# Optimization experiments

Measured on AMD Instinct MI355X. Metric: run time of the kernel, lower is better.

The kernel has to match this reference:

```python
import jax, jax.numpy as jnp
import numpy as np

DIM = 256
HEADS = 8
SR = 2
EPS = 1e-5


def setup_inputs() -> dict:
    key = jax.random.key(0)
    ks = jax.random.split(key, 8)
    B, N, C = 4, 4096, DIM
    s = 0.02
    return {
        "x": jax.random.normal(ks[0], (B, N, C), dtype=jnp.float32),
        "H": 64,
        "W": 64,
        # sequence-reduction conv (Conv2d dim->dim, k=SR, stride=SR), OIHW
        "sr_w": jax.random.normal(ks[1], (C, C, SR, SR), dtype=jnp.float32) * s,
        "sr_b": jnp.zeros((C,), dtype=jnp.float32),
        "ln_g": jnp.ones((C,), dtype=jnp.float32),
        "ln_b": jnp.zeros((C,), dtype=jnp.float32),
        # torch Linear weights: y = x @ W.T (qkv_bias=False)
        "q_w": jax.random.normal(ks[2], (C, C), dtype=jnp.float32) * s,
        "kv_w": jax.random.normal(ks[3], (2 * C, C), dtype=jnp.float32) * s,
        "proj_w": jax.random.normal(ks[4], (C, C), dtype=jnp.float32) * s,
        "proj_b": jnp.zeros((C,), dtype=jnp.float32),
    }


def reference(x, H, W, sr_w, sr_b, ln_g, ln_b, q_w, kv_w, proj_w, proj_b):
    B, N, C = x.shape
    h, d = HEADS, C // HEADS
    scale = d ** -0.5

    # q: [B, h, N, d]
    q = (x @ q_w.T).reshape(B, N, h, d).transpose(0, 2, 1, 3)

    # sequence reduction: [B,N,C] -> [B,C,H,W] -> conv(k=SR, s=SR) -> [B, N', C]
    x_ = x.transpose(0, 2, 1).reshape(B, C, H, W)
    x_ = jax.lax.conv_general_dilated(
        x_, sr_w, window_strides=(SR, SR), padding="VALID",
        dimension_numbers=("NCHW", "OIHW", "NCHW"))
    x_ = x_ + sr_b[None, :, None, None]
    x_ = x_.reshape(B, C, -1).transpose(0, 2, 1)  # [B, N', C]

    # LayerNorm over C
    mu = x_.mean(-1, keepdims=True)
    var = x_.var(-1, keepdims=True)
    x_ = (x_ - mu) * jax.lax.rsqrt(var + EPS) * ln_g + ln_b

    # kv: [2, B, h, N', d]
    kv = (x_ @ kv_w.T).reshape(B, -1, 2, h, d).transpose(2, 0, 3, 1, 4)
    k, v = kv[0], kv[1]

    attn = jnp.einsum("bhnd,bhmd->bhnm", q, k) * scale
    attn = jax.nn.softmax(attn, axis=-1)  # attn_drop = 0 -> identity
    out = jnp.einsum("bhnm,bhmd->bhnd", attn, v)
    out = out.transpose(0, 2, 1, 3).reshape(B, N, C)

    return out @ proj_w.T + proj_b  # proj_drop = 0 -> identity
```

## Files before the change

kernel.cpp:

```cpp
#include <hip/hip_runtime.h>
#include <hip/hip_bf16.h>


typedef __attribute__((ext_vector_type(8))) short bf16x8;
typedef __attribute__((ext_vector_type(8))) unsigned short u16x8;
typedef __attribute__((ext_vector_type(4))) float f32x4;
typedef __attribute__((ext_vector_type(16))) float f32x16;
typedef __attribute__((ext_vector_type(2))) unsigned u32x2v;
typedef __attribute__((ext_vector_type(4))) unsigned u32x4v;

__device__ inline unsigned short f2bf(float f) {
  unsigned u = __float_as_uint(f);
  u += 0x7fffu + ((u >> 16) & 1u);
  return (unsigned short)(u >> 16);
}

__device__ inline u16x8 cast8(float4 a, float4 b) {
  u16x8 r;
  r[0] = f2bf(a.x); r[1] = f2bf(a.y); r[2] = f2bf(a.z); r[3] = f2bf(a.w);
  r[4] = f2bf(b.x); r[5] = f2bf(b.y); r[6] = f2bf(b.z); r[7] = f2bf(b.w);
  return r;
}

__global__ __launch_bounds__(256) void prep_kernel(
    const float* __restrict__ srw, unsigned short* __restrict__ srw_bf) {
  const int o = blockIdx.x, t = threadIdx.x;
  float4 v = reinterpret_cast<const float4*>(srw + (size_t)o * 1024)[t];
  srw_bf[(size_t)o * 1024 + 0 * 256 + t] = f2bf(v.x);
  srw_bf[(size_t)o * 1024 + 1 * 256 + t] = f2bf(v.y);
  srw_bf[(size_t)o * 1024 + 2 * 256 + t] = f2bf(v.z);
  srw_bf[(size_t)o * 1024 + 3 * 256 + t] = f2bf(v.w);
}

__device__ __forceinline__ void gemm_body_q(
    const float* __restrict__ Af, const float* __restrict__ W,
    unsigned short* __restrict__ C, float oscale,
    int m0, int n0, unsigned short* Asb, unsigned short* Bsb) {
  const int K = 256, N = 256, NK = 8;
  const int tid = threadIdx.x;
  const int w = tid >> 6, l = tid & 63, c = l & 15, g = l >> 4;
  const int wr = w >> 1, wc = w & 1;
  const int ar = tid >> 1, ah = tid & 1;
  const int bn = tid >> 2, bq = tid & 3;
  const int ABUF = 128 * 40, BBUF = 64 * 40;

  const float* aptr = Af + (size_t)(m0 + ar) * K + ah * 16;
  const float* wptr = W + (size_t)(n0 + bn) * K + bq * 8;

  f32x4 acc[4][2];
#pragma unroll
  for (int mt = 0; mt < 4; ++mt)
#pragma unroll
    for (int nt = 0; nt < 2; ++nt)
#pragma unroll
      for (int r = 0; r < 4; ++r) acc[mt][nt][r] = 0.f;

  {
    float4 a0 = *reinterpret_cast<const float4*>(aptr);
    float4 a1 = *reinterpret_cast<const float4*>(aptr + 4);
    float4 a2 = *reinterpret_cast<const float4*>(aptr + 8);
    float4 a3 = *reinterpret_cast<const float4*>(aptr + 12);
    float4 w0 = *reinterpret_cast<const float4*>(wptr);
    float4 w1 = *reinterpret_cast<const float4*>(wptr + 4);
    *reinterpret_cast<u16x8*>(&Asb[ar * 40 + ah * 16]) = cast8(a0, a1);
    *reinterpret_cast<u16x8*>(&Asb[ar * 40 + ah * 16 + 8]) = cast8(a2, a3);
    *reinterpret_cast<u16x8*>(&Bsb[bn * 40 + bq * 8]) = cast8(w0, w1);
  }

  for (int t = 0; t < NK; ++t) {
    const int cur = t & 1;
    __syncthreads();
    float4 na0, na1, na2, na3, nw0, nw1;
    if (t < NK - 1) {
      const float* ap = aptr + (t + 1) * 32;
      na0 = *reinterpret_cast<const float4*>(ap);
      na1 = *reinterpret_cast<const float4*>(ap + 4);
      na2 = *reinterpret_cast<const float4*>(ap + 8);
      na3 = *reinterpret_cast<const float4*>(ap + 12);
      const float* wp = wptr + (t + 1) * 32;
      nw0 = *reinterpret_cast<const float4*>(wp);
      nw1 = *reinterpret_cast<const float4*>(wp + 4);
    }
    bf16x8 af[4], bfr[2];
#pragma unroll
    for (int mt = 0; mt < 4; ++mt)
      af[mt] = *reinterpret_cast<const bf16x8*>(
          &Asb[cur * ABUF + (wr * 64 + mt * 16 + c) * 40 + g * 8]);
#pragma unroll
    for (int nt = 0; nt < 2; ++nt)
      bfr[nt] = *reinterpret_cast<const bf16x8*>(
          &Bsb[cur * BBUF + (wc * 32 + nt * 16 + c) * 40 + g * 8]);
#pragma unroll
    for (int mt = 0; mt < 4; ++mt)
#pragma unroll
      for (int nt = 0; nt < 2; ++nt)
        acc[mt][nt] = __builtin_amdgcn_mfma_f32_16x16x32_bf16(
            af[mt], bfr[nt], acc[mt][nt], 0, 0, 0);
    if (t < NK - 1) {
      const int nxt = cur ^ 1;
      *reinterpret_cast<u16x8*>(&Asb[nxt * ABUF + ar * 40 + ah * 16]) = cast8(na0, na1);
      *reinterpret_cast<u16x8*>(&Asb[nxt * ABUF + ar * 40 + ah * 16 + 8]) = cast8(na2, na3);
      *reinterpret_cast<u16x8*>(&Bsb[nxt * BBUF + bn * 40 + bq * 8]) = cast8(nw0, nw1);
    }
  }

#pragma unroll
  for (int mt = 0; mt < 4; ++mt)
#pragma unroll
    for (int nt = 0; nt < 2; ++nt) {
      int row = m0 + wr * 64 + mt * 16 + g * 4;
      int col = n0 + wc * 32 + nt * 16 + c;
#pragma unroll
      for (int r = 0; r < 4; ++r)
        C[(size_t)(row + r) * N + col] = f2bf(acc[mt][nt][r] * oscale);
    }
}

__device__ __forceinline__ void conv_body(
    const float* __restrict__ Xf, const unsigned short* __restrict__ Wp,
    const float* __restrict__ bias, float* __restrict__ C,
    int m0, int n0, unsigned short* Asb, unsigned short* Bsb) {
  const int NK = 32;
  const int tid = threadIdx.x;
  const int w = tid >> 6, l = tid & 63, c = l & 15, g = l >> 4;
  const int wr = w >> 1, wc = w & 1;
  const int sr = tid >> 2, sh = tid & 3;
  const int BUF = 64 * 40;

  int base[4];
  {
    int row = m0 + sr;
    int b = row >> 10, o = row & 1023, oh = o >> 5, ow = o & 31;
#pragma unroll
    for (int tap = 0; tap < 4; ++tap) {
      int n = ((oh << 1) + (tap >> 1)) * 64 + (ow << 1) + (tap & 1);
      base[tap] = ((b << 12) + n) << 8;
    }
  }
  const unsigned short* wptr = Wp + (size_t)(n0 + sr) * 1024 + sh * 8;

  f32x4 acc[2][2];
#pragma unroll
  for (int mt = 0; mt < 2; ++mt)
#pragma unroll
    for (int nt = 0; nt < 2; ++nt)
#pragma unroll
      for (int r = 0; r < 4; ++r) acc[mt][nt][r] = 0.f;

  {
    const float* xp = Xf + base[0] + sh * 8;
    float4 a0 = *reinterpret_cast<const float4*>(xp);
    float4 a1 = *reinterpret_cast<const float4*>(xp + 4);
    *reinterpret_cast<u16x8*>(&Asb[sr * 40 + sh * 8]) = cast8(a0, a1);
    *reinterpret_cast<u16x8*>(&Bsb[sr * 40 + sh * 8]) =
        *reinterpret_cast<const u16x8*>(wptr);
  }

  for (int t = 0; t < NK; ++t) {
    const int cur = t & 1;
    __syncthreads();
    float4 na0, na1; u16x8 nw;
    if (t < NK - 1) {
      const int k0n = (t + 1) * 32;
      const float* xp = Xf + base[k0n >> 8] + (k0n & 255) + sh * 8;
      na0 = *reinterpret_cast<const float4*>(xp);
      na1 = *reinterpret_cast<const float4*>(xp + 4);
      nw = *reinterpret_cast<const u16x8*>(wptr + (t + 1) * 32);
    }
    bf16x8 af[2], bfr[2];
#pragma unroll
    for (int mt = 0; mt < 2; ++mt)
      af[mt] = *reinterpret_cast<const bf16x8*>(
          &Asb[cur * BUF + (wr * 32 + mt * 16 + c) * 40 + g * 8]);
#pragma unroll
    for (int nt = 0; nt < 2; ++nt)
      bfr[nt] = *reinterpret_cast<const bf16x8*>(
          &Bsb[cur * BUF + (wc * 32 + nt * 16 + c) * 40 + g * 8]);
#pragma unroll
    for (int mt = 0; mt < 2; ++mt)
#pragma unroll
      for (int nt = 0; nt < 2; ++nt)
        acc[mt][nt] = __builtin_amdgcn_mfma_f32_16x16x32_bf16(
            af[mt], bfr[nt], acc[mt][nt], 0, 0, 0);
    if (t < NK - 1) {
      const int nxt = cur ^ 1;
      *reinterpret_cast<u16x8*>(&Asb[nxt * BUF + sr * 40 + sh * 8]) = cast8(na0, na1);
      *reinterpret_cast<u16x8*>(&Bsb[nxt * BUF + sr * 40 + sh * 8]) = nw;
    }
  }

#pragma unroll
  for (int mt = 0; mt < 2; ++mt)
#pragma unroll
    for (int nt = 0; nt < 2; ++nt) {
      int row = m0 + wr * 32 + mt * 16 + g * 4;
      int col = n0 + wc * 32 + nt * 16 + c;
      float bv = bias[col];
#pragma unroll
      for (int r = 0; r < 4; ++r)
        C[(size_t)(row + r) * 256 + col] = acc[mt][nt][r] + bv;
    }
}

__global__ __launch_bounds__(256) void qconv_kernel(
    const float* __restrict__ x, const float* __restrict__ q_w,
    unsigned short* __restrict__ q_bf, const unsigned short* __restrict__ srw_bf,
    const float* __restrict__ sr_b, float* __restrict__ xred, float qscale) {
  __shared__ unsigned short smem[2 * 128 * 40 + 2 * 64 * 40];
  const int bid = blockIdx.x;
  if (bid < 512) {
    gemm_body_q(x, q_w, q_bf, qscale,
                (bid >> 2) * 128, (bid & 3) * 64, smem, smem + 2 * 128 * 40);
  } else {
    int cb = bid - 512;
    conv_body(x, srw_bf, sr_b, xred,
              (cb >> 2) * 64, (cb & 3) * 64, smem, smem + 2 * 64 * 40);
  }
}

__global__ __launch_bounds__(256) void kv_gemm(
    const unsigned short* __restrict__ A, const float* __restrict__ W,
    unsigned short* __restrict__ Kb, unsigned short* __restrict__ Vtp) {
  __shared__ unsigned short Asb[2 * 128 * 40];
  __shared__ unsigned short Bsb[2 * 64 * 40];
  const int K = 256, NK = 8;
  const int tid = threadIdx.x;
  const int w = tid >> 6, l = tid & 63, c = l & 15, g = l >> 4;
  const int wr = w >> 1, wc = w & 1;
  const int m0 = blockIdx.y * 128, n0 = blockIdx.x * 64;
  const int ar = tid >> 1, ah = tid & 1;
  const int bn = tid >> 2, bq = tid & 3;
  const int ABUF = 128 * 40, BBUF = 64 * 40;

  const unsigned short* aptr = A + (size_t)(m0 + ar) * K + ah * 16;
  const float* wptr = W + (size_t)(n0 + bn) * K + bq * 8;

  f32x4 acc[4][2];
#pragma unroll
  for (int mt = 0; mt < 4; ++mt)
#pragma unroll
    for (int nt = 0; nt < 2; ++nt)
#pragma unroll
      for (int r = 0; r < 4; ++r) acc[mt][nt][r] = 0.f;

  {
    u16x8 a0 = *reinterpret_cast<const u16x8*>(aptr);
    u16x8 a1 = *reinterpret_cast<const u16x8*>(aptr + 8);
    float4 w0 = *reinterpret_cast<const float4*>(wptr);
    float4 w1 = *reinterpret_cast<const float4*>(wptr + 4);
    *reinterpret_cast<u16x8*>(&Asb[ar * 40 + ah * 16]) = a0;
    *reinterpret_cast<u16x8*>(&Asb[ar * 40 + ah * 16 + 8]) = a1;
    *reinterpret_cast<u16x8*>(&Bsb[bn * 40 + bq * 8]) = cast8(w0, w1);
  }

  for (int t = 0; t < NK; ++t) {
    const int cur = t & 1;
    __syncthreads();
    u16x8 na0, na1; float4 nw0, nw1;
    if (t < NK - 1) {
      const unsigned short* ap = aptr + (t + 1) * 32;
      na0 = *reinterpret_cast<const u16x8*>(ap);
      na1 = *reinterpret_cast<const u16x8*>(ap + 8);
      const float* wp = wptr + (t + 1) * 32;
      nw0 = *reinterpret_cast<const float4*>(wp);
      nw1 = *reinterpret_cast<const float4*>(wp + 4);
    }
    bf16x8 af[4], bfr[2];
#pragma unroll
    for (int mt = 0; mt < 4; ++mt)
      af[mt] = *reinterpret_cast<const bf16x8*>(
          &Asb[cur * ABUF + (wr * 64 + mt * 16 + c) * 40 + g * 8]);
#pragma unroll
    for (int nt = 0; nt < 2; ++nt)
      bfr[nt] = *reinterpret_cast<const bf16x8*>(
          &Bsb[cur * BBUF + (wc * 32 + nt * 16 + c) * 40 + g * 8]);
#pragma unroll
    for (int mt = 0; mt < 4; ++mt)
#pragma unroll
      for (int nt = 0; nt < 2; ++nt)
        acc[mt][nt] = __builtin_amdgcn_mfma_f32_16x16x32_bf16(
            af[mt], bfr[nt], acc[mt][nt], 0, 0, 0);
    if (t < NK - 1) {
      const int nxt = cur ^ 1;
      *reinterpret_cast<u16x8*>(&Asb[nxt * ABUF + ar * 40 + ah * 16]) = na0;
      *reinterpret_cast<u16x8*>(&Asb[nxt * ABUF + ar * 40 + ah * 16 + 8]) = na1;
      *reinterpret_cast<u16x8*>(&Bsb[nxt * BBUF + bn * 40 + bq * 8]) = cast8(nw0, nw1);
    }
  }

#pragma unroll
  for (int mt = 0; mt < 4; ++mt)
#pragma unroll
    for (int nt = 0; nt < 2; ++nt) {
      int row = m0 + wr * 64 + mt * 16 + g * 4;
      int col = n0 + wc * 32 + nt * 16 + c;
#pragma unroll
      for (int r = 0; r < 4; ++r) {
        float v = acc[mt][nt][r];
        if (col < 256) {
          Kb[(size_t)(row + r) * 256 + col] = f2bf(v);
        } else {
          int head = (col - 256) >> 5, d = (col - 256) & 31;
          int rr = row + r;
          Vtp[((size_t)(((rr >> 10) << 3) + head) * 32 + d) * 1024 +
              (rr & 1023)] = f2bf(v);
        }
      }
    }
}

__global__ __launch_bounds__(256) void proj_gemm(
    const unsigned short* __restrict__ A, const float* __restrict__ W,
    const float* __restrict__ bias, float* __restrict__ C) {
  __shared__ unsigned short Asb[2 * 64 * 40];
  __shared__ unsigned short Bsb[2 * 64 * 40];
  const int NK = 8;
  const int tid = threadIdx.x;
  const int w = tid >> 6, l = tid & 63, c = l & 15, g = l >> 4;
  const int wr = w >> 1, wc = w & 1;
  const int m0 = blockIdx.y * 64, n0 = blockIdx.x * 64;
  const int sr = tid >> 2, sh = tid & 3;
  const int BUF = 64 * 40;

  const unsigned short* aptr = A + (size_t)(m0 + sr) * 256 + sh * 8;
  const float* wptr = W + (size_t)(n0 + sr) * 256 + sh * 8;

  f32x4 acc[2][2];
#pragma unroll
  for (int mt = 0; mt < 2; ++mt)
#pragma unroll
    for (int nt = 0; nt < 2; ++nt)
#pragma unroll
      for (int r = 0; r < 4; ++r) acc[mt][nt][r] = 0.f;

  {
    u16x8 av = *reinterpret_cast<const u16x8*>(aptr);
    float4 w0 = *reinterpret_cast<const float4*>(wptr);
    float4 w1 = *reinterpret_cast<const float4*>(wptr + 4);
    *reinterpret_cast<u16x8*>(&Asb[sr * 40 + sh * 8]) = av;
    *reinterpret_cast<u16x8*>(&Bsb[sr * 40 + sh * 8]) = cast8(w0, w1);
  }

  for (int t = 0; t < NK; ++t) {
    const int cur = t & 1;
    __syncthreads();
    u16x8 na; float4 nw0, nw1;
    if (t < NK - 1) {
      na = *reinterpret_cast<const u16x8*>(aptr + (t + 1) * 32);
      const float* wp = wptr + (t + 1) * 32;
      nw0 = *reinterpret_cast<const float4*>(wp);
      nw1 = *reinterpret_cast<const float4*>(wp + 4);
    }
    bf16x8 af[2], bfr[2];
#pragma unroll
    for (int mt = 0; mt < 2; ++mt)
      af[mt] = *reinterpret_cast<const bf16x8*>(
          &Asb[cur * BUF + (wr * 32 + mt * 16 + c) * 40 + g * 8]);
#pragma unroll
    for (int nt = 0; nt < 2; ++nt)
      bfr[nt] = *reinterpret_cast<const bf16x8*>(
          &Bsb[cur * BUF + (wc * 32 + nt * 16 + c) * 40 + g * 8]);
#pragma unroll
    for (int mt = 0; mt < 2; ++mt)
#pragma unroll
      for (int nt = 0; nt < 2; ++nt)
        acc[mt][nt] = __builtin_amdgcn_mfma_f32_16x16x32_bf16(
            af[mt], bfr[nt], acc[mt][nt], 0, 0, 0);
    if (t < NK - 1) {
      const int nxt = cur ^ 1;
      *reinterpret_cast<u16x8*>(&Asb[nxt * BUF + sr * 40 + sh * 8]) = na;
      *reinterpret_cast<u16x8*>(&Bsb[nxt * BUF + sr * 40 + sh * 8]) = cast8(nw0, nw1);
    }
  }

#pragma unroll
  for (int mt = 0; mt < 2; ++mt)
#pragma unroll
    for (int nt = 0; nt < 2; ++nt) {
      int row = m0 + wr * 32 + mt * 16 + g * 4;
      int col = n0 + wc * 32 + nt * 16 + c;
      float bv = bias[col];
#pragma unroll
      for (int r = 0; r < 4; ++r)
        C[(size_t)(row + r) * 256 + col] = acc[mt][nt][r] + bv;
    }
}

__global__ __launch_bounds__(256) void ln_kernel(
    const float* __restrict__ xr, const float* __restrict__ gam,
    const float* __restrict__ bet, unsigned short* __restrict__ xo) {
  const int w = threadIdx.x >> 6, l = threadIdx.x & 63;
  const int row = blockIdx.x * 4 + w;
  float4 v = *reinterpret_cast<const float4*>(xr + (size_t)row * 256 + l * 4);
  float s = (v.x + v.y) + (v.z + v.w);
  float s2 = (v.x * v.x + v.y * v.y) + (v.z * v.z + v.w * v.w);
#pragma unroll
  for (int off = 32; off > 0; off >>= 1) {
    s  += __shfl_xor(s, off, 64);
    s2 += __shfl_xor(s2, off, 64);
  }
  float mean = s * (1.f / 256.f);
  float var = s2 * (1.f / 256.f) - mean * mean;
  float rstd = rsqrtf(var + 1e-5f);
  float4 g = *reinterpret_cast<const float4*>(gam + l * 4);
  float4 bb = *reinterpret_cast<const float4*>(bet + l * 4);
  unsigned short o0 = f2bf((v.x - mean) * rstd * g.x + bb.x);
  unsigned short o1 = f2bf((v.y - mean) * rstd * g.y + bb.y);
  unsigned short o2 = f2bf((v.z - mean) * rstd * g.z + bb.z);
  unsigned short o3 = f2bf((v.w - mean) * rstd * g.w + bb.w);
  unsigned long long pk =
      (unsigned long long)o0 | ((unsigned long long)o1 << 16) |
      ((unsigned long long)o2 << 32) | ((unsigned long long)o3 << 48);
  *reinterpret_cast<unsigned long long*>(xo + (size_t)row * 256 + l * 4) = pk;
}

__global__ __launch_bounds__(256) void attn_mfma(
    const unsigned short* __restrict__ Qb,
    const unsigned short* __restrict__ Kb,
    const unsigned short* __restrict__ Vtg,
    unsigned short* __restrict__ O) {
  __shared__ __align__(16) unsigned short Kt[2][64][36];
  __shared__ __align__(16) unsigned short Vt[2][32][72];

  const int tid = threadIdx.x;
  const int l = tid & 63;
  const int w = tid >> 6;
  const int q32 = l & 31, hi = l >> 5;
  const int wg = blockIdx.x;
  const int qb = wg & 31, head = (wg >> 5) & 7, b = wg >> 8;
  const int hcol = head << 5;
  const int q0 = (b << 12) + (qb << 7) + (w << 5);

  bf16x8 qf[2];
  {
    const unsigned short* qp = Qb + (size_t)(q0 + q32) * 256 + hcol + hi * 8;
    qf[0] = *reinterpret_cast<const bf16x8*>(qp);
    qf[1] = *reinterpret_cast<const bf16x8*>(qp + 16);
  }

  const int sd = tid >> 3, skv = (tid & 7) << 3;
  const unsigned short* vtrow =
      Vtg + ((size_t)((b << 3) + head) * 32 + sd) * 1024 + skv;
  const int kr = tid >> 2, kh = (tid & 3) << 3;
  const unsigned short* ktrow =
      Kb + ((size_t)(b << 10) + kr) * 256 + hcol + kh;

  {
    u16x8 va = *reinterpret_cast<const u16x8*>(vtrow);
    *reinterpret_cast<u16x8*>(&Vt[0][sd][skv]) = va;
    u16x8 ka = *reinterpret_cast<const u16x8*>(ktrow);
    *reinterpret_cast<u16x8*>(&Kt[0][kr][kh]) = ka;
  }

  f32x16 acc;
#pragma unroll
  for (int r = 0; r < 16; ++r) acc[r] = 0.f;
  float lsum = 0.f;

  for (int t = 0; t < 16; ++t) {
    const int cur = t & 1;
    __syncthreads();

    u16x8 nv0, nk0;
    if (t < 15) {
      nv0 = *reinterpret_cast<const u16x8*>(vtrow + (t + 1) * 64);
      nk0 = *reinterpret_cast<const u16x8*>(ktrow + (size_t)(t + 1) * 64 * 256);
    }

    f32x16 s[2];
    {
      bf16x8 k00 = *reinterpret_cast<const bf16x8*>(&Kt[cur][q32][hi * 8]);
      bf16x8 k01 = *reinterpret_cast<const bf16x8*>(&Kt[cur][q32][hi * 8 + 16]);
      bf16x8 k10 = *reinterpret_cast<const bf16x8*>(&Kt[cur][q32 + 32][hi * 8]);
      bf16x8 k11 = *reinterpret_cast<const bf16x8*>(&Kt[cur][q32 + 32][hi * 8 + 16]);
      f32x16 z;
#pragma unroll
      for (int r = 0; r < 16; ++r) z[r] = 0.f;
      s[0] = __builtin_amdgcn_mfma_f32_32x32x16_bf16(k00, qf[0], z, 0, 0, 0);
      s[0] = __builtin_amdgcn_mfma_f32_32x32x16_bf16(k01, qf[1], s[0], 0, 0, 0);
      s[1] = __builtin_amdgcn_mfma_f32_32x32x16_bf16(k10, qf[0], z, 0, 0, 0);
      s[1] = __builtin_amdgcn_mfma_f32_32x32x16_bf16(k11, qf[1], s[1], 0, 0, 0);
    }

#pragma unroll
    for (int kvb = 0; kvb < 2; ++kvb) {
      float p16[16];
#pragma unroll
      for (int r = 0; r < 16; ++r)
        p16[r] = __builtin_amdgcn_exp2f(s[kvb][r]);
      float s0 = (p16[0] + p16[1]) + (p16[2] + p16[3]);
      float s1 = (p16[4] + p16[5]) + (p16[6] + p16[7]);
      float s2 = (p16[8] + p16[9]) + (p16[10] + p16[11]);
      float s3 = (p16[12] + p16[13]) + (p16[14] + p16[15]);
      lsum += (s0 + s1) + (s2 + s3);
      unsigned A[8];
#pragma unroll
      for (int i = 0; i < 8; ++i) {
        unsigned o;
        asm("v_cvt_pk_bf16_f32 %0, %1, %2"
            : "=v"(o) : "v"(p16[2 * i]), "v"(p16[2 * i + 1]));
        A[i] = o;
      }
      u32x2v r02 = __builtin_amdgcn_permlane32_swap(A[0], A[2], false, false);
      u32x2v r13 = __builtin_amdgcn_permlane32_swap(A[1], A[3], false, false);
      u32x2v r46 = __builtin_amdgcn_permlane32_swap(A[4], A[6], false, false);
      u32x2v r57 = __builtin_amdgcn_permlane32_swap(A[5], A[7], false, false);
      u32x4v pk0 = {r02[0], r13[0], r02[1], r13[1]};
      u32x4v pk1 = {r46[0], r57[0], r46[1], r57[1]};
      bf16x8 pf0 = __builtin_bit_cast(bf16x8, pk0);
      bf16x8 pf1 = __builtin_bit_cast(bf16x8, pk1);
      const unsigned short* vrow = &Vt[cur][q32][kvb * 32 + hi * 8];
      bf16x8 vf0 = *reinterpret_cast<const bf16x8*>(vrow);
      bf16x8 vf1 = *reinterpret_cast<const bf16x8*>(vrow + 16);
      acc = __builtin_amdgcn_mfma_f32_32x32x16_bf16(vf0, pf0, acc, 0, 0, 0);
      acc = __builtin_amdgcn_mfma_f32_32x32x16_bf16(vf1, pf1, acc, 0, 0, 0);
    }

    if (t < 15) {
      *reinterpret_cast<u16x8*>(&Vt[cur ^ 1][sd][skv]) = nv0;
      *reinterpret_cast<u16x8*>(&Kt[cur ^ 1][kr][kh]) = nk0;
    }
  }

  lsum += __shfl_xor(lsum, 32, 64);
  float inv = 1.f / lsum;
  unsigned short* orow = O + (size_t)(q0 + q32) * 256 + hcol;
#pragma unroll
  for (int rb = 0; rb < 4; ++rb) {
    const int d0 = rb * 8 + hi * 4;
    float a0 = acc[rb * 4 + 0] * inv, a1 = acc[rb * 4 + 1] * inv;
    float a2 = acc[rb * 4 + 2] * inv, a3 = acc[rb * 4 + 3] * inv;
    unsigned w0, w1;
    asm("v_cvt_pk_bf16_f32 %0, %1, %2" : "=v"(w0) : "v"(a0), "v"(a1));
    asm("v_cvt_pk_bf16_f32 %0, %1, %2" : "=v"(w1) : "v"(a2), "v"(a3));
    unsigned long long pk = (unsigned long long)w0 | ((unsigned long long)w1 << 32);
    *reinterpret_cast<unsigned long long*>(orow + d0) = pk;
  }
}

extern "C" void kernel_launch(void* const* d_in, const int* in_sizes, int n_in,
                              void* d_out, int out_size, void* d_ws,
                              size_t ws_size, hipStream_t stream) {
  const float* x      = (const float*)d_in[0];
  const float* sr_w   = (const float*)d_in[3];
  const float* sr_b   = (const float*)d_in[4];
  const float* ln_g   = (const float*)d_in[5];
  const float* ln_b   = (const float*)d_in[6];
  const float* q_w    = (const float*)d_in[7];
  const float* kv_w   = (const float*)d_in[8];
  const float* proj_w = (const float*)d_in[9];
  const float* proj_b = (const float*)d_in[10];
  float* out = (float*)d_out;

  char* ws = (char*)d_ws;
  unsigned short* q_bf    = (unsigned short*)(ws);
  unsigned short* srw_bf  = (unsigned short*)(ws + 8388608);
  float*          xred    = (float*)(ws + 8912896);
  unsigned short* x_ln    = (unsigned short*)(ws + 13107200);
  unsigned short* k_buf   = (unsigned short*)(ws + 15204352);
  unsigned short* vt_buf  = (unsigned short*)(ws + 17301504);
  unsigned short* attn_bf = (unsigned short*)(ws + 19398656);

  const float qscale = 0.25506975154985854f;

  prep_kernel<<<256, 256, 0, stream>>>(sr_w, srw_bf);
  qconv_kernel<<<768, 256, 0, stream>>>(
      x, q_w, q_bf, srw_bf, sr_b, xred, qscale);
  ln_kernel<<<1024, 256, 0, stream>>>(xred, ln_g, ln_b, x_ln);
  kv_gemm<<<dim3(8, 32), 256, 0, stream>>>(x_ln, kv_w, k_buf, vt_buf);
  attn_mfma<<<1024, 256, 0, stream>>>(q_bf, k_buf, vt_buf, attn_bf);
  proj_gemm<<<dim3(4, 256), 256, 0, stream>>>(attn_bf, proj_w, proj_b, out);
}
```

Baseline: 88.79 us.

## Split attention KV range across wave pairs and merge partial sums in LDS

Each attention workgroup now handles 64 queries instead of 128, with two wave pairs each covering half of the 1024 keys. The partial accumulators and row sums are combined through LDS at the end. K fragments are now read directly from global memory instead of being staged in LDS. The grid doubles to 2048 blocks to increase parallelism and shorten each block's serial KV loop. In exchange, K traffic is no longer shared through LDS, and the final merge adds LDS traffic plus an extra barrier. The merge skips max-rescaling because the kernel already uses unnormalized exp without a running max.

After: 101.6 us. 1.14x slower.

```diff
diff --git a/kernel.cpp b/kernel.cpp
--- a/kernel.cpp
+++ b/kernel.cpp
@@ -419,17 +419,17 @@
     const unsigned short* __restrict__ Kb,
     const unsigned short* __restrict__ Vtg,
     unsigned short* __restrict__ O) {
-  __shared__ __align__(16) unsigned short Kt[2][64][36];
-  __shared__ __align__(16) unsigned short Vt[2][32][72];
+  __shared__ __align__(16) unsigned short Vt[2][2][32][72];
 
   const int tid = threadIdx.x;
   const int l = tid & 63;
   const int w = tid >> 6;
   const int q32 = l & 31, hi = l >> 5;
+  const int half = w >> 1;
   const int wg = blockIdx.x;
-  const int qb = wg & 31, head = (wg >> 5) & 7, b = wg >> 8;
+  const int qb = wg & 63, head = (wg >> 6) & 7, b = wg >> 9;
   const int hcol = head << 5;
-  const int q0 = (b << 12) + (qb << 7) + (w << 5);
+  const int q0 = (b << 12) + (qb << 6) + ((w & 1) << 5);
 
   bf16x8 qf[2];
   {
@@ -438,18 +438,19 @@
     qf[1] = *reinterpret_cast<const bf16x8*>(qp + 16);
   }
 
-  const int sd = tid >> 3, skv = (tid & 7) << 3;
+  const int hid = tid & 127;
+  const int sd = hid >> 2, skv = (hid & 3) << 4;
   const unsigned short* vtrow =
-      Vtg + ((size_t)((b << 3) + head) * 32 + sd) * 1024 + skv;
-  const int kr = tid >> 2, kh = (tid & 3) << 3;
-  const unsigned short* ktrow =
-      Kb + ((size_t)(b << 10) + kr) * 256 + hcol + kh;
+      Vtg + ((size_t)((b << 3) + head) * 32 + sd) * 1024 + (half << 9) + skv;
+
+  const unsigned short* kbase0 =
+      Kb + ((size_t)((b << 10) + (half << 9) + q32)) * 256 + hcol + hi * 8;
 
   {
     u16x8 va = *reinterpret_cast<const u16x8*>(vtrow);
-    *reinterpret_cast<u16x8*>(&Vt[0][sd][skv]) = va;
-    u16x8 ka = *reinterpret_cast<const u16x8*>(ktrow);
-    *reinterpret_cast<u16x8*>(&Kt[0][kr][kh]) = ka;
+    u16x8 vb = *reinterpret_cast<const u16x8*>(vtrow + 8);
+    *reinterpret_cast<u16x8*>(&Vt[half][0][sd][skv]) = va;
+    *reinterpret_cast<u16x8*>(&Vt[half][0][sd][skv + 8]) = vb;
   }
 
   f32x16 acc;
@@ -457,22 +458,24 @@
   for (int r = 0; r < 16; ++r) acc[r] = 0.f;
   float lsum = 0.f;
 
-  for (int t = 0; t < 16; ++t) {
+  for (int t = 0; t < 8; ++t) {
     const int cur = t & 1;
     __syncthreads();
 
-    u16x8 nv0, nk0;
-    if (t < 15) {
-      nv0 = *reinterpret_cast<const u16x8*>(vtrow + (t + 1) * 64);
-      nk0 = *reinterpret_cast<const u16x8*>(ktrow + (size_t)(t + 1) * 64 * 256);
-    }
-
+    u16x8 nv0, nv1;
+    if (t < 7) {
+      const unsigned short* vp = vtrow + (t + 1) * 64;
+      nv0 = *reinterpret_cast<const u16x8*>(vp);
+      nv1 = *reinterpret_cast<const u16x8*>(vp + 8);
+    }
+
+    const unsigned short* kbase = kbase0 + (size_t)t * 64 * 256;
     f32x16 s[2];
     {
-      bf16x8 k00 = *reinterpret_cast<const bf16x8*>(&Kt[cur][q32][hi * 8]);
-      bf16x8 k01 = *reinterpret_cast<const bf16x8*>(&Kt[cur][q32][hi * 8 + 16]);
-      bf16x8 k10 = *reinterpret_cast<const bf16x8*>(&Kt[cur][q32 + 32][hi * 8]);
-      bf16x8 k11 = *reinterpret_cast<const bf16x8*>(&Kt[cur][q32 + 32][hi * 8 + 16]);
+      bf16x8 k00 = *reinterpret_cast<const bf16x8*>(kbase);
+      bf16x8 k01 = *reinterpret_cast<const bf16x8*>(kbase + 16);
+      bf16x8 k10 = *reinterpret_cast<const bf16x8*>(kbase + 32 * 256);
+      bf16x8 k11 = *reinterpret_cast<const bf16x8*>(kbase + 32 * 256 + 16);
       f32x16 z;
 #pragma unroll
       for (int r = 0; r < 16; ++r) z[r] = 0.f;
@@ -509,32 +512,58 @@
       u32x4v pk1 = {r46[0], r57[0], r46[1], r57[1]};
       bf16x8 pf0 = __builtin_bit_cast(bf16x8, pk0);
       bf16x8 pf1 = __builtin_bit_cast(bf16x8, pk1);
-      const unsigned short* vrow = &Vt[cur][q32][kvb * 32 + hi * 8];
+      const unsigned short* vrow = &Vt[half][cur][q32][kvb * 32 + hi * 8];
       bf16x8 vf0 = *reinterpret_cast<const bf16x8*>(vrow);
       bf16x8 vf1 = *reinterpret_cast<const bf16x8*>(vrow + 16);
       acc = __builtin_amdgcn_mfma_f32_32x32x16_bf16(vf0, pf0, acc, 0, 0, 0);
       acc = __builtin_amdgcn_mfma_f32_32x32x16_bf16(vf1, pf1, acc, 0, 0, 0);
     }
 
-    if (t < 15) {
-      *reinterpret_cast<u16x8*>(&Vt[cur ^ 1][sd][skv]) = nv0;
-      *reinterpret_cast<u16x8*>(&Kt[cur ^ 1][kr][kh]) = nk0;
+    if (t < 7) {
+      *reinterpret_cast<u16x8*>(&Vt[half][cur ^ 1][sd][skv]) = nv0;
+      *reinterpret_cast<u16x8*>(&Vt[half][cur ^ 1][sd][skv + 8]) = nv1;
     }
   }
 
   lsum += __shfl_xor(lsum, 32, 64);
-  float inv = 1.f / lsum;
-  unsigned short* orow = O + (size_t)(q0 + q32) * 256 + hcol;
-#pragma unroll
-  for (int rb = 0; rb < 4; ++rb) {
-    const int d0 = rb * 8 + hi * 4;
-    float a0 = acc[rb * 4 + 0] * inv, a1 = acc[rb * 4 + 1] * inv;
-    float a2 = acc[rb * 4 + 2] * inv, a3 = acc[rb * 4 + 3] * inv;
-    unsigned w0, w1;
-    asm("v_cvt_pk_bf16_f32 %0, %1, %2" : "=v"(w0) : "v"(a0), "v"(a1));
-    asm("v_cvt_pk_bf16_f32 %0, %1, %2" : "=v"(w1) : "v"(a2), "v"(a3));
-    unsigned long long pk = (unsigned long long)w0 | ((unsigned long long)w1 << 32);
-    *reinterpret_cast<unsigned long long*>(orow + d0) = pk;
+
+  __syncthreads();
+  float* Ob = reinterpret_cast<float*>(&Vt[0][0][0][0]);
+  float* Lb = Ob + 2 * 4 * 64 * 4;
+  if (w >= 2) {
+    const int wi = w - 2;
+#pragma unroll
+    for (int rc = 0; rc < 4; ++rc) {
+      f32x4 chunk;
+      chunk[0] = acc[rc * 4 + 0]; chunk[1] = acc[rc * 4 + 1];
+      chunk[2] = acc[rc * 4 + 2]; chunk[3] = acc[rc * 4 + 3];
+      *reinterpret_cast<f32x4*>(&Ob[((wi * 4 + rc) * 64 + l) * 4]) = chunk;
+    }
+    if (hi == 0) Lb[wi * 32 + q32] = lsum;
+  }
+  __syncthreads();
+  if (w < 2) {
+#pragma unroll
+    for (int rc = 0; rc < 4; ++rc) {
+      f32x4 chunk = *reinterpret_cast<const f32x4*>(
+          &Ob[((w * 4 + rc) * 64 + l) * 4]);
+      acc[rc * 4 + 0] += chunk[0]; acc[rc * 4 + 1] += chunk[1];
+      acc[rc * 4 + 2] += chunk[2]; acc[rc * 4 + 3] += chunk[3];
+    }
+    lsum += Lb[w * 32 + q32];
+    float inv = 1.f / lsum;
+    unsigned short* orow = O + (size_t)(q0 + q32) * 256 + hcol;
+#pragma unroll
+    for (int rb = 0; rb < 4; ++rb) {
+      const int d0 = rb * 8 + hi * 4;
+      float a0 = acc[rb * 4 + 0] * inv, a1 = acc[rb * 4 + 1] * inv;
+      float a2 = acc[rb * 4 + 2] * inv, a3 = acc[rb * 4 + 3] * inv;
+      unsigned w0, w1;
+      asm("v_cvt_pk_bf16_f32 %0, %1, %2" : "=v"(w0) : "v"(a0), "v"(a1));
+      asm("v_cvt_pk_bf16_f32 %0, %1, %2" : "=v"(w1) : "v"(a2), "v"(a3));
+      unsigned long long pk = (unsigned long long)w0 | ((unsigned long long)w1 << 32);
+      *reinterpret_cast<unsigned long long*>(orow + d0) = pk;
+    }
   }
 }
 
@@ -568,6 +597,6 @@
       x, q_w, q_bf, srw_bf, sr_b, xred, qscale);
   ln_kernel<<<1024, 256, 0, stream>>>(xred, ln_g, ln_b, x_ln);
   kv_gemm<<<dim3(8, 32), 256, 0, stream>>>(x_ln, kv_w, k_buf, vt_buf);
-  attn_mfma<<<1024, 256, 0, stream>>>(q_bf, k_buf, vt_buf, attn_bf);
+  attn_mfma<<<2048, 256, 0, stream>>>(q_bf, k_buf, vt_buf, attn_bf);
   proj_gemm<<<dim3(4, 256), 256, 0, stream>>>(attn_bf, proj_w, proj_b, out);
 }
```

## Fuse LayerNorm into KV GEMM, fold gamma/beta into weights, shrink Q tiles

Applied to the files above, without the earlier changes.

Removes the separate LayerNorm kernel. The KV GEMM now computes per-row mean and rstd from the fp32 conv output and normalizes while staging A into shared memory. The LN gamma is folded into a prepacked bf16 KV weight, and beta becomes a precomputed output bias, both produced in the prep kernel. The Q projection tiles shrink from 128x64 to 64x64, doubling the block count for better load balance alongside the conv blocks. The cost is an extra pass over the reduced activations in each KV block to get row statistics, and fp32 A loads where bf16 ones were used before.

New measurement: 96.06 us. 8.2% more time.

```diff
diff --git a/kernel.cpp b/kernel.cpp
--- a/kernel.cpp
+++ b/kernel.cpp
@@ -22,34 +22,58 @@
   return r;
 }
 
+__device__ inline u16x8 lncast8(float4 a, float4 b, float mean, float rstd) {
+  u16x8 r;
+  r[0] = f2bf((a.x - mean) * rstd); r[1] = f2bf((a.y - mean) * rstd);
+  r[2] = f2bf((a.z - mean) * rstd); r[3] = f2bf((a.w - mean) * rstd);
+  r[4] = f2bf((b.x - mean) * rstd); r[5] = f2bf((b.y - mean) * rstd);
+  r[6] = f2bf((b.z - mean) * rstd); r[7] = f2bf((b.w - mean) * rstd);
+  return r;
+}
+
 __global__ __launch_bounds__(256) void prep_kernel(
-    const float* __restrict__ srw, unsigned short* __restrict__ srw_bf) {
-  const int o = blockIdx.x, t = threadIdx.x;
-  float4 v = reinterpret_cast<const float4*>(srw + (size_t)o * 1024)[t];
-  srw_bf[(size_t)o * 1024 + 0 * 256 + t] = f2bf(v.x);
-  srw_bf[(size_t)o * 1024 + 1 * 256 + t] = f2bf(v.y);
-  srw_bf[(size_t)o * 1024 + 2 * 256 + t] = f2bf(v.z);
-  srw_bf[(size_t)o * 1024 + 3 * 256 + t] = f2bf(v.w);
-}
-
-__device__ __forceinline__ void gemm_body_q(
+    const float* __restrict__ srw, unsigned short* __restrict__ srw_bf,
+    const float* __restrict__ kvw, const float* __restrict__ ln_g,
+    const float* __restrict__ ln_b, unsigned short* __restrict__ kvw_bf,
+    float* __restrict__ bias2) {
+  __shared__ float red[4];
+  const int bid = blockIdx.x, t = threadIdx.x;
+  if (bid < 256) {
+    const int o = bid;
+    float4 v = reinterpret_cast<const float4*>(srw + (size_t)o * 1024)[t];
+    srw_bf[(size_t)o * 1024 + 0 * 256 + t] = f2bf(v.x);
+    srw_bf[(size_t)o * 1024 + 1 * 256 + t] = f2bf(v.y);
+    srw_bf[(size_t)o * 1024 + 2 * 256 + t] = f2bf(v.z);
+    srw_bf[(size_t)o * 1024 + 3 * 256 + t] = f2bf(v.w);
+  } else {
+    const int o = bid - 256;
+    float wv = kvw[(size_t)o * 256 + t];
+    kvw_bf[(size_t)o * 256 + t] = f2bf(wv * ln_g[t]);
+    float p = wv * ln_b[t];
+#pragma unroll
+    for (int off = 32; off > 0; off >>= 1) p += __shfl_xor(p, off, 64);
+    if ((t & 63) == 0) red[t >> 6] = p;
+    __syncthreads();
+    if (t == 0) bias2[o] = (red[0] + red[1]) + (red[2] + red[3]);
+  }
+}
+
+__device__ __forceinline__ void gemm_body_q64(
     const float* __restrict__ Af, const float* __restrict__ W,
     unsigned short* __restrict__ C, float oscale,
     int m0, int n0, unsigned short* Asb, unsigned short* Bsb) {
-  const int K = 256, N = 256, NK = 8;
+  const int NK = 8, BUF = 64 * 40;
   const int tid = threadIdx.x;
   const int w = tid >> 6, l = tid & 63, c = l & 15, g = l >> 4;
   const int wr = w >> 1, wc = w & 1;
-  const int ar = tid >> 1, ah = tid & 1;
-  const int bn = tid >> 2, bq = tid & 3;
-  const int ABUF = 128 * 40, BBUF = 64 * 40;
-
-  const float* aptr = Af + (size_t)(m0 + ar) * K + ah * 16;
-  const float* wptr = W + (size_t)(n0 + bn) * K + bq * 8;
-
-  f32x4 acc[4][2];
-#pragma unroll
-  for (int mt = 0; mt < 4; ++mt)
+  const int sr = tid >> 2, sh = tid & 3;
+
+  const float* aptr = Af + (size_t)(m0 + sr) * 256 + sh * 8;
+  const float* wptr = W + (size_t)(n0 + sr) * 256 + sh * 8;
+
+  f32x4 acc[2][2];
+#pragma unroll
+  for (int mt = 0; mt < 2; ++mt)
 #pragma unroll
     for (int nt = 0; nt < 2; ++nt)
 #pragma unroll
@@ -58,61 +82,55 @@
   {
     float4 a0 = *reinterpret_cast<const float4*>(aptr);
     float4 a1 = *reinterpret_cast<const float4*>(aptr + 4);
-    float4 a2 = *reinterpret_cast<const float4*>(aptr + 8);
-    float4 a3 = *reinterpret_cast<const float4*>(aptr + 12);
     float4 w0 = *reinterpret_cast<const float4*>(wptr);
     float4 w1 = *reinterpret_cast<const float4*>(wptr + 4);
-    *reinterpret_cast<u16x8*>(&Asb[ar * 40 + ah * 16]) = cast8(a0, a1);
-    *reinterpret_cast<u16x8*>(&Asb[ar * 40 + ah * 16 + 8]) = cast8(a2, a3);
-    *reinterpret_cast<u16x8*>(&Bsb[bn * 40 + bq * 8]) = cast8(w0, w1);
+    *reinterpret_cast<u16x8*>(&Asb[sr * 40 + sh * 8]) = cast8(a0, a1);
+    *reinterpret_cast<u16x8*>(&Bsb[sr * 40 + sh * 8]) = cast8(w0, w1);
   }
 
   for (int t = 0; t < NK; ++t) {
     const int cur = t & 1;
     __syncthreads();
-    float4 na0, na1, na2, na3, nw0, nw1;
+    float4 na0, na1, nw0, nw1;
     if (t < NK - 1) {
       const float* ap = aptr + (t + 1) * 32;
       na0 = *reinterpret_cast<const float4*>(ap);
       na1 = *reinterpret_cast<const float4*>(ap + 4);
-      na2 = *reinterpret_cast<const float4*>(ap + 8);
-      na3 = *reinterpret_cast<const float4*>(ap + 12);
       const float* wp = wptr + (t + 1) * 32;
       nw0 = *reinterpret_cast<const float4*>(wp);
       nw1 = *reinterpret_cast<const float4*>(wp + 4);
     }
-    bf16x8 af[4], bfr[2];
-#pragma unroll
-    for (int mt = 0; mt < 4; ++mt)
+    bf16x8 af[2], bfr[2];
+#pragma unroll
+    for (int mt = 0; mt < 2; ++mt)
       af[mt] = *reinterpret_cast<const bf16x8*>(
-          &Asb[cur * ABUF + (wr * 64 + mt * 16 + c) * 40 + g * 8]);
+          &Asb[cur * BUF + (wr * 32 + mt * 16 + c) * 40 + g * 8]);
 #pragma unroll
     for (int nt = 0; nt < 2; ++nt)
       bfr[nt] = *reinterpret_cast<const bf16x8*>(
-          &Bsb[cur * BBUF + (wc * 32 + nt * 16 + c) * 40 + g * 8]);
-#pragma unroll
-    for (int mt = 0; mt < 4; ++mt)
+          &Bsb[cur * BUF + (wc * 32 + nt * 16 + c) * 40 + g * 8]);
+#pragma unroll
+    for (int mt = 0; mt < 2; ++mt)
 #pragma unroll
       for (int nt = 0; nt < 2; ++nt)
         acc[mt][nt] = __builtin_amdgcn_mfma_f32_16x16x32_bf16(
             af[mt], bfr[nt], acc[mt][nt], 0, 0, 0);
     if (t < NK - 1) {
       const int nxt = cur ^ 1;
-      *reinterpret_cast<u16x8*>(&Asb[nxt * ABUF + ar * 40 + ah * 16]) = cast8(na0, na1);
-      *reinterpret_cast<u16x8*>(&Asb[nxt * ABUF + ar * 40 + ah * 16 + 8]) = cast8(na2, na3);
-      *reinterpret_cast<u16x8*>(&Bsb[nxt * BBUF + bn * 40 + bq * 8]) = cast8(nw0, nw1);
-    }
-  }
-
-#pragma unroll
-  for (int mt = 0; mt < 4; ++mt)
+      *reinterpret_cast<u16x8*>(&Asb[nxt * BUF + sr * 40 + sh * 8]) = cast8(na0, na1);
+      *reinterpret_cast<u16x8*>(&Bsb[nxt * BUF + sr * 40 + sh * 8]) = cast8(nw0, nw1);
+    }
+  }
+
+#pragma unroll
+  for (int mt = 0; mt < 2; ++mt)
 #pragma unroll
     for (int nt = 0; nt < 2; ++nt) {
-      int row = m0 + wr * 64 + mt * 16 + g * 4;
+      int row = m0 + wr * 32 + mt * 16 + g * 4;
       int col = n0 + wc * 32 + nt * 16 + c;
 #pragma unroll
       for (int r = 0; r < 4; ++r)
-        C[(size_t)(row + r) * N + col] = f2bf(acc[mt][nt][r] * oscale);
+        C[(size_t)(row + r) * 256 + col] = f2bf(acc[mt][nt][r] * oscale);
     }
 }
 
@@ -206,24 +224,26 @@
     const float* __restrict__ x, const float* __restrict__ q_w,
     unsigned short* __restrict__ q_bf, const unsigned short* __restrict__ srw_bf,
     const float* __restrict__ sr_b, float* __restrict__ xred, float qscale) {
-  __shared__ unsigned short smem[2 * 128 * 40 + 2 * 64 * 40];
+  __shared__ unsigned short smem[4 * 64 * 40];
   const int bid = blockIdx.x;
-  if (bid < 512) {
-    gemm_body_q(x, q_w, q_bf, qscale,
-                (bid >> 2) * 128, (bid & 3) * 64, smem, smem + 2 * 128 * 40);
+  if (bid < 1024) {
+    gemm_body_q64(x, q_w, q_bf, qscale,
+                  (bid >> 2) * 64, (bid & 3) * 64, smem, smem + 2 * 64 * 40);
   } else {
-    int cb = bid - 512;
+    int cb = bid - 1024;
     conv_body(x, srw_bf, sr_b, xred,
               (cb >> 2) * 64, (cb & 3) * 64, smem, smem + 2 * 64 * 40);
   }
 }
 
 __global__ __launch_bounds__(256) void kv_gemm(
-    const unsigned short* __restrict__ A, const float* __restrict__ W,
+    const float* __restrict__ Xr, const unsigned short* __restrict__ Wb,
+    const float* __restrict__ bias2,
     unsigned short* __restrict__ Kb, unsigned short* __restrict__ Vtp) {
   __shared__ unsigned short Asb[2 * 128 * 40];
   __shared__ unsigned short Bsb[2 * 64 * 40];
-  const int K = 256, NK = 8;
+  __shared__ float Mu[128], Rs[128];
+  const int NK = 8;
   const int tid = threadIdx.x;
   const int w = tid >> 6, l = tid & 63, c = l & 15, g = l >> 4;
   const int wr = w >> 1, wc = w & 1;
@@ -232,8 +252,29 @@
   const int bn = tid >> 2, bq = tid & 3;
   const int ABUF = 128 * 40, BBUF = 64 * 40;
 
-  const unsigned short* aptr = A + (size_t)(m0 + ar) * K + ah * 16;
-  const float* wptr = W + (size_t)(n0 + bn) * K + bq * 8;
+  {
+    const float* xp = Xr + (size_t)(m0 + ar) * 256 + ah * 128;
+    float s = 0.f, s2 = 0.f;
+#pragma unroll
+    for (int i = 0; i < 32; ++i) {
+      float4 v = reinterpret_cast<const float4*>(xp)[i];
+      s += (v.x + v.y) + (v.z + v.w);
+      s2 += (v.x * v.x + v.y * v.y) + (v.z * v.z + v.w * v.w);
+    }
+    s += __shfl_xor(s, 1, 64);
+    s2 += __shfl_xor(s2, 1, 64);
+    if (ah == 0) {
+      float mean = s * (1.f / 256.f);
+      float var = s2 * (1.f / 256.f) - mean * mean;
+      Mu[ar] = mean;
+      Rs[ar] = rsqrtf(var + 1e-5f);
+    }
+  }
+  __syncthreads();
+  const float mean = Mu[ar], rstd = Rs[ar];
+
+  const float* aptr = Xr + (size_t)(m0 + ar) * 256 + ah * 16;
+  const unsigned short* wptr = Wb + (size_t)(n0 + bn) * 256 + bq * 8;
 
   f32x4 acc[4][2];
 #pragma unroll
@@ -244,26 +285,27 @@
       for (int r = 0; r < 4; ++r) acc[mt][nt][r] = 0.f;
 
   {
-    u16x8 a0 = *reinterpret_cast<const u16x8*>(aptr);
-    u16x8 a1 = *reinterpret_cast<const u16x8*>(aptr + 8);
-    float4 w0 = *reinterpret_cast<const float4*>(wptr);
-    float4 w1 = *reinterpret_cast<const float4*>(wptr + 4);
-    *reinterpret_cast<u16x8*>(&Asb[ar * 40 + ah * 16]) = a0;
-    *reinterpret_cast<u16x8*>(&Asb[ar * 40 + ah * 16 + 8]) = a1;
-    *reinterpret_cast<u16x8*>(&Bsb[bn * 40 + bq * 8]) = cast8(w0, w1);
+    float4 a0 = *reinterpret_cast<const float4*>(aptr);
+    float4 a1 = *reinterpret_cast<const float4*>(aptr + 4);
+    float4 a2 = *reinterpret_cast<const float4*>(aptr + 8);
+    float4 a3 = *reinterpret_cast<const float4*>(aptr + 12);
+    *reinterpret_cast<u16x8*>(&Asb[ar * 40 + ah * 16]) = lncast8(a0, a1, mean, rstd);
+    *reinterpret_cast<u16x8*>(&Asb[ar * 40 + ah * 16 + 8]) = lncast8(a2, a3, mean, rstd);
+    *reinterpret_cast<u16x8*>(&Bsb[bn * 40 + bq * 8]) =
+        *reinterpret_cast<const u16x8*>(wptr);
   }
 
   for (int t = 0; t < NK; ++t) {
     const int cur = t & 1;
     __syncthreads();
-    u16x8 na0, na1; float4 nw0, nw1;
-    if (t < NK - 1) {
-      const unsigned short* ap = aptr + (t + 1) * 32;
-      na0 = *reinterpret_cast<const u16x8*>(ap);
-      na1 = *reinterpret_cast<const u16x8*>(ap + 8);
-      const float* wp = wptr + (t + 1) * 32;
-      nw0 = *reinterpret_cast<const float4*>(wp);
-      nw1 = *reinterpret_cast<const float4*>(wp + 4);
+    float4 na0, na1, na2, na3; u16x8 nw;
+    if (t < NK - 1) {
+      const float* ap = aptr + (t + 1) * 32;
+      na0 = *reinterpret_cast<const float4*>(ap);
+      na1 = *reinterpret_cast<const float4*>(ap + 4);
+      na2 = *reinterpret_cast<const float4*>(ap + 8);
+      na3 = *reinterpret_cast<const float4*>(ap + 12);
+      nw = *reinterpret_cast<const u16x8*>(wptr + (t + 1) * 32);
     }
     bf16x8 af[4], bfr[2];
 #pragma unroll
@@ -282,9 +324,11 @@
             af[mt], bfr[nt], acc[mt][nt], 0, 0, 0);
     if (t < NK - 1) {
       const int nxt = cur ^ 1;
-      *reinterpret_cast<u16x8*>(&Asb[nxt * ABUF + ar * 40 + ah * 16]) = na0;
-      *reinterpret_cast<u16x8*>(&Asb[nxt * ABUF + ar * 40 + ah * 16 + 8]) = na1;
-      *reinterpret_cast<u16x8*>(&Bsb[nxt * BBUF + bn * 40 + bq * 8]) = cast8(nw0, nw1);
+      *reinterpret_cast<u16x8*>(&Asb[nxt * ABUF + ar * 40 + ah * 16]) =
+          lncast8(na0, na1, mean, rstd);
+      *reinterpret_cast<u16x8*>(&Asb[nxt * ABUF + ar * 40 + ah * 16 + 8]) =
+          lncast8(na2, na3, mean, rstd);
+      *reinterpret_cast<u16x8*>(&Bsb[nxt * BBUF + bn * 40 + bq * 8]) = nw;
     }
   }
 
@@ -294,9 +338,10 @@
     for (int nt = 0; nt < 2; ++nt) {
       int row = m0 + wr * 64 + mt * 16 + g * 4;
       int col = n0 + wc * 32 + nt * 16 + c;
+      float bv = bias2[col];
 #pragma unroll
       for (int r = 0; r < 4; ++r) {
-        float v = acc[mt][nt][r];
+        float v = acc[mt][nt][r] + bv;
         if (col < 256) {
           Kb[(size_t)(row + r) * 256 + col] = f2bf(v);
         } else {
@@ -384,34 +429,6 @@
       for (int r = 0; r < 4; ++r)
         C[(size_t)(row + r) * 256 + col] = acc[mt][nt][r] + bv;
     }
-}
-
-__global__ __launch_bounds__(256) void ln_kernel(
-    const float* __restrict__ xr, const float* __restrict__ gam,
-    const float* __restrict__ bet, unsigned short* __restrict__ xo) {
-  const int w = threadIdx.x >> 6, l = threadIdx.x & 63;
-  const int row = blockIdx.x * 4 + w;
-  float4 v = *reinterpret_cast<const float4*>(xr + (size_t)row * 256 + l * 4);
-  float s = (v.x + v.y) + (v.z + v.w);
-  float s2 = (v.x * v.x + v.y * v.y) + (v.z * v.z + v.w * v.w);
-#pragma unroll
-  for (int off = 32; off > 0; off >>= 1) {
-    s  += __shfl_xor(s, off, 64);
-    s2 += __shfl_xor(s2, off, 64);
-  }
-  float mean = s * (1.f / 256.f);
-  float var = s2 * (1.f / 256.f) - mean * mean;
-  float rstd = rsqrtf(var + 1e-5f);
-  float4 g = *reinterpret_cast<const float4*>(gam + l * 4);
-  float4 bb = *reinterpret_cast<const float4*>(bet + l * 4);
-  unsigned short o0 = f2bf((v.x - mean) * rstd * g.x + bb.x);
-  unsigned short o1 = f2bf((v.y - mean) * rstd * g.y + bb.y);
-  unsigned short o2 = f2bf((v.z - mean) * rstd * g.z + bb.z);
-  unsigned short o3 = f2bf((v.w - mean) * rstd * g.w + bb.w);
-  unsigned long long pk =
-      (unsigned long long)o0 | ((unsigned long long)o1 << 16) |
-      ((unsigned long long)o2 << 32) | ((unsigned long long)o3 << 48);
-  *reinterpret_cast<unsigned long long*>(xo + (size_t)row * 256 + l * 4) = pk;
 }
 
 __global__ __launch_bounds__(256) void attn_mfma(
@@ -556,18 +573,19 @@
   unsigned short* q_bf    = (unsigned short*)(ws);
   unsigned short* srw_bf  = (unsigned short*)(ws + 8388608);
   float*          xred    = (float*)(ws + 8912896);
-  unsigned short* x_ln    = (unsigned short*)(ws + 13107200);
-  unsigned short* k_buf   = (unsigned short*)(ws + 15204352);
-  unsigned short* vt_buf  = (unsigned short*)(ws + 17301504);
-  unsigned short* attn_bf = (unsigned short*)(ws + 19398656);
+  unsigned short* kvw_bf  = (unsigned short*)(ws + 13107200);
+  float*          bias2   = (float*)(ws + 13369344);
+  unsigned short* k_buf   = (unsigned short*)(ws + 13371392);
+  unsigned short* vt_buf  = (unsigned short*)(ws + 15468544);
+  unsigned short* attn_bf = (unsigned short*)(ws + 17565696);
 
   const float qscale = 0.25506975154985854f;
 
-  prep_kernel<<<256, 256, 0, stream>>>(sr_w, srw_bf);
-  qconv_kernel<<<768, 256, 0, stream>>>(
+  prep_kernel<<<768, 256, 0, stream>>>(
+      sr_w, srw_bf, kv_w, ln_g, ln_b, kvw_bf, bias2);
+  qconv_kernel<<<1280, 256, 0, stream>>>(
       x, q_w, q_bf, srw_bf, sr_b, xred, qscale);
-  ln_kernel<<<1024, 256, 0, stream>>>(xred, ln_g, ln_b, x_ln);
-  kv_gemm<<<dim3(8, 32), 256, 0, stream>>>(x_ln, kv_w, k_buf, vt_buf);
+  kv_gemm<<<dim3(8, 32), 256, 0, stream>>>(xred, kvw_bf, bias2, k_buf, vt_buf);
   attn_mfma<<<1024, 256, 0, stream>>>(q_bf, k_buf, vt_buf, attn_bf);
   proj_gemm<<<dim3(4, 256), 256, 0, stream>>>(attn_bf, proj_w, proj_b, out);
 }
```
